# Performance work log

Measured on AMD Instinct MI355X. Metric: run time of the kernel, lower is better.

## Reference

```python
import jax, jax.numpy as jnp
import numpy as np

N = 200000
EPS = 1e-6

def _build_indices():
    # irreps = 128x0e + 64x1e + 32x2e, mirroring MySeperableLayerNorm.__init__ bookkeeping
    scalar_idx = np.arange(128)                       # positions of 0e scalars
    scalar_ch = np.arange(128)                        # their channel ids
    vector_idx = np.arange(128, 480)                  # positions of vector components
    vector_ch_local = np.concatenate([
        np.repeat(np.arange(64), 3),
        np.repeat(np.arange(64, 96), 5),
    ])
    ch_expand = np.concatenate([
        np.arange(128),                               # scalar channels 0..127
        np.repeat(np.arange(128, 192), 3),            # 1e channels 128..191
        np.repeat(np.arange(192, 224), 5),            # 2e channels 192..223
    ])
    return scalar_idx, scalar_ch, vector_idx, vector_ch_local, ch_expand

def setup_inputs() -> dict:
    key = jax.random.key(0)
    ks = jax.random.split(key, 8)
    si, sc, vi, vcl, ce = _build_indices()
    f32 = jnp.float32
    inp = {
        "x": jax.random.normal(ks[0], (N, 480), dtype=f32),
        "W1": jax.random.normal(ks[1], (56, 224), dtype=f32) * 0.05,
        "b1": jax.random.normal(ks[2], (56,), dtype=f32) * 0.05,
        "W2": jax.random.normal(ks[3], (224, 56), dtype=f32) * 0.05,
        "b2": jax.random.normal(ks[4], (224,), dtype=f32) * 0.05,
        "aff_w": 1.0 + 0.1 * jax.random.normal(ks[5], (1, 224), dtype=f32),
        "aff_b": 0.1 * jax.random.normal(ks[6], (1, 128), dtype=f32),
        "scalar_idx": jnp.asarray(si, jnp.int32),
        "scalar_ch": jnp.asarray(sc, jnp.int32),
        "vector_idx": jnp.asarray(vi, jnp.int32),
        "vector_ch_local": jnp.asarray(vcl, jnp.int32),
        "ch_expand": jnp.asarray(ce, jnp.int32),
    }
    return inp

def reference(x, W1, b1, W2, b2, aff_w, aff_b,
              scalar_idx, scalar_ch, vector_idx, vector_ch_local, ch_expand):
    n = x.shape[0]
    num_features = W2.shape[0]
    num_scalar = scalar_idx.shape[0]
    num_vector = num_features - num_scalar

    # --- invariants ---
    scalars = x[:, scalar_idx]                                   # [N, S]
    scalars_centered = scalars - scalars.mean(axis=1, keepdims=True)
    vec_sq = x[:, vector_idx] ** 2                               # [N, Vdim]
    # scatter_mean over vector components -> per-vector mean square
    sums = jnp.zeros((n, num_vector), x.dtype).at[:, vector_ch_local].add(vec_sq)
    counts = jnp.zeros((num_vector,), x.dtype).at[vector_ch_local].add(1.0)
    vectors_rms = jnp.sqrt(sums / counts + EPS)                  # [N, V]

    feats = jnp.concatenate([scalars_centered, vectors_rms], axis=1)  # [N, S+V]
    # gate_norm == 'rms'
    feats = feats * jax.lax.rsqrt(jnp.mean(feats ** 2, axis=1, keepdims=True) + EPS)

    # --- gating MLP (Linear -> SiLU -> Linear) ---
    h = jax.nn.silu(feats @ W1.T + b1)                           # [N, H]
    gate = jax.nn.sigmoid(h @ W2.T + b2) * aff_w                 # [N, C]

    # --- scatter-affine expansion ---
    x_out = x * gate[:, ch_expand]                               # [N, D]
    x_out = x_out.at[:, scalar_idx].set(scalars_centered * gate[:, scalar_ch] + aff_b)
    return x_out
```

## Files before the change

kernel.cpp:

```cpp
#include <hip/hip_runtime.h>

typedef __bf16 bf16;
typedef bf16 bf16x8 __attribute__((ext_vector_type(8)));
typedef float f32x4 __attribute__((ext_vector_type(4)));

#define EPS 1e-6f


__global__ __launch_bounds__(256, 4) void fused(
    const float* __restrict__ x,
    const float* __restrict__ b1v, const float* __restrict__ b2v,
    const float* __restrict__ aw,  const float* __restrict__ ab,
    const bf16* __restrict__ W1b,  const bf16* __restrict__ W2b,
    float* __restrict__ out)
{
    __shared__ unsigned char smem[4 * 7488];
    const int tid = threadIdx.x;
    const int wv  = tid >> 6;
    const int l   = tid & 63;
    const int q   = l >> 4;
    const int c   = l & 15;
    unsigned char* reg = smem + wv * 7488;
    bf16*  feats = (bf16*)reg;
    bf16*  Hs    = (bf16*)reg;
    bf16*  gateb = (bf16*)reg;
    float* srow  = (float*)(reg + 7424);
    const int r0 = blockIdx.x * 64 + wv * 16;

    float cen0[16], cen1[16];
    #pragma unroll
    for (int b = 0; b < 4; ++b) {
        float v0[4], v1[4], t0[4], t1[4], t2[4], p0[4], p1[4], p2[4], p3[4], p4[4];
        #pragma unroll
        for (int j = 0; j < 4; ++j) {
            const float* xr = x + (r0 + 4 * b + j) * 480;
            v0[j] = xr[l];
            v1[j] = xr[64 + l];
            t0[j] = xr[128 + 3 * l];
            t1[j] = xr[129 + 3 * l];
            t2[j] = xr[130 + 3 * l];
            if (l < 32) {
                const float* pp = xr + 320 + 5 * l;
                p0[j] = pp[0]; p1[j] = pp[1]; p2[j] = pp[2]; p3[j] = pp[3]; p4[j] = pp[4];
            }
        }
        #pragma unroll
        for (int j = 0; j < 4; ++j) {
            const int i = 4 * b + j;
            float su = v0[j] + v1[j];
            #pragma unroll
            for (int m = 1; m < 64; m <<= 1) su += __shfl_xor(su, m);
            const float mean = su * (1.0f / 128.0f);
            const float c0 = v0[j] - mean, c1 = v1[j] - mean;
            cen0[i] = c0; cen1[i] = c1;

            const float ra = sqrtf((t0[j]*t0[j] + t1[j]*t1[j] + t2[j]*t2[j]) * (1.0f / 3.0f) + EPS);
            float rb = 0.0f;
            if (l < 32) {
                const float g5 = p0[j]*p0[j] + p1[j]*p1[j] + p2[j]*p2[j] + p3[j]*p3[j] + p4[j]*p4[j];
                rb = sqrtf(g5 * 0.2f + EPS);
            }

            bf16* fr = feats + i * 232;
            fr[l]       = (bf16)c0;
            fr[64 + l]  = (bf16)c1;
            fr[128 + l] = (bf16)ra;
            if (l < 32) fr[192 + l] = (bf16)rb;

            float ms = c0 * c0 + c1 * c1 + ra * ra + rb * rb;
            #pragma unroll
            for (int m = 1; m < 64; m <<= 1) ms += __shfl_xor(ms, m);
            if (l == 0) srow[i] = rsqrtf(ms * (1.0f / 224.0f) + EPS);
        }
    }
    __builtin_amdgcn_wave_barrier();

    bf16x8 af[7];
    {
        const bf16* frow = feats + c * 232;
        #pragma unroll
        for (int ks = 0; ks < 7; ++ks)
            af[ks] = *(const bf16x8*)(frow + ks * 32 + q * 8);
    }
    __builtin_amdgcn_wave_barrier();
    #pragma unroll
    for (int t = 0; t < 4; ++t) {
        f32x4 acc = {0.f, 0.f, 0.f, 0.f};
        const int n = t * 16 + c;
        const bf16* wrow = W1b + n * 224 + q * 8;
        #pragma unroll
        for (int ks = 0; ks < 7; ++ks)
            acc = __builtin_amdgcn_mfma_f32_16x16x32_bf16(
                      af[ks], *(const bf16x8*)(wrow + ks * 32), acc, 0, 0, 0);
        float bb = 0.f;
        if (n < 56) bb = b1v[n];
        #pragma unroll
        for (int r = 0; r < 4; ++r) {
            const int row = q * 4 + r;
            const float z = acc[r] * srow[row] + bb;
            float hv = 0.f;
            if (n < 56) hv = z / (1.f + __expf(-z));
            Hs[row * 72 + n] = (bf16)hv;
        }
    }
    __builtin_amdgcn_wave_barrier();

    const bf16x8 ha0 = *(const bf16x8*)(Hs + c * 72 + q * 8);
    const bf16x8 ha1 = *(const bf16x8*)(Hs + c * 72 + 32 + q * 8);
    __builtin_amdgcn_wave_barrier();
    #pragma unroll
    for (int t = 0; t < 14; ++t) {
        f32x4 acc = {0.f, 0.f, 0.f, 0.f};
        const int nn = t * 16 + c;
        const bf16* wrow = W2b + nn * 64 + q * 8;
        acc = __builtin_amdgcn_mfma_f32_16x16x32_bf16(ha0, *(const bf16x8*)(wrow),      acc, 0, 0, 0);
        acc = __builtin_amdgcn_mfma_f32_16x16x32_bf16(ha1, *(const bf16x8*)(wrow + 32), acc, 0, 0, 0);
        const float bb = b2v[nn];
        const float a  = aw[nn];
        #pragma unroll
        for (int r = 0; r < 4; ++r) {
            const int row = q * 4 + r;
            const float g = a / (1.f + __expf(-(acc[r] + bb)));
            gateb[row * 225 + nn] = (bf16)g;
        }
    }
    __builtin_amdgcn_wave_barrier();

    const float ab0 = ab[l], ab1 = ab[64 + l];
    #pragma unroll
    for (int i = 0; i < 16; ++i) {
        const int base = (r0 + i) * 480;
        const bf16* gr = gateb + i * 225;
        out[base + l]      = cen0[i] * (float)gr[l]      + ab0;
        out[base + 64 + l] = cen1[i] * (float)gr[64 + l] + ab1;
        #pragma unroll
        for (int k = 0; k < 6; ++k) {
            const int cc = 128 + 64 * k + l;
            if (cc < 480) {
                const int d  = cc - 128;
                const int ch = (d < 192) ? (128 + d / 3) : (192 + (d - 192) / 5);
                out[base + cc] = x[base + cc] * (float)gr[ch];
            }
        }
    }
}

__global__ __launch_bounds__(256) void convert_w(
    const float* __restrict__ W1, const float* __restrict__ W2,
    bf16* __restrict__ W1b, bf16* __restrict__ W2b)
{
    const int t = blockIdx.x * 256 + threadIdx.x;
    if (t < 64 * 224) {
        const int n = t / 224, k = t % 224;
        W1b[t] = (n < 56) ? (bf16)W1[n * 224 + k] : (bf16)0.f;
    } else {
        const int u = t - 64 * 224;
        const int n = u >> 6, kk = u & 63;
        W2b[u] = (kk < 56) ? (bf16)W2[n * 56 + kk] : (bf16)0.f;
    }
}

extern "C" void kernel_launch(void* const* d_in, const int* in_sizes, int n_in,
                              void* d_out, int out_size, void* d_ws, size_t ws_size,
                              hipStream_t stream) {
    const float* x  = (const float*)d_in[0];
    const float* W1 = (const float*)d_in[1];
    const float* b1 = (const float*)d_in[2];
    const float* W2 = (const float*)d_in[3];
    const float* b2 = (const float*)d_in[4];
    const float* aw = (const float*)d_in[5];
    const float* ab = (const float*)d_in[6];
    bf16* W1b = (bf16*)d_ws;
    bf16* W2b = W1b + 64 * 224;
    const int rows = in_sizes[0] / 480;
    convert_w<<<112, 256, 0, stream>>>(W1, W2, W1b, W2b);
    fused<<<rows / 64, 256, 0, stream>>>(x, b1, b2, aw, ab, W1b, W2b, (float*)d_out);
}
```

Baseline: 786.4 us.

## Vectorize row loads/stores with 16-lane-per-row mapping and software prefetch

```diff
diff --git a/kernel.cpp b/kernel.cpp
--- a/kernel.cpp
+++ b/kernel.cpp
@@ -2,12 +2,49 @@
 
 typedef __bf16 bf16;
 typedef bf16 bf16x8 __attribute__((ext_vector_type(8)));
+typedef bf16 bf16x4v __attribute__((ext_vector_type(4)));
+typedef bf16 bf16x2v __attribute__((ext_vector_type(2)));
 typedef float f32x4 __attribute__((ext_vector_type(4)));
 
 #define EPS 1e-6f
 
 
-__global__ __launch_bounds__(256, 4) void fused(
+struct XR { float4 s0, s1, t0, t1, t2; float2 u0, u1, u2, u3, u4; };
+struct XE { float4 a0, a1, a2; float2 b0, b1, b2, b3, b4; };
+
+__device__ __forceinline__ XR ldrow(const float* __restrict__ xr, int c) {
+    XR r;
+    r.s0 = *(const float4*)(xr + 8 * c);
+    r.s1 = *(const float4*)(xr + 8 * c + 4);
+    const float* tp = xr + 128 + 12 * c;
+    r.t0 = *(const float4*)(tp);
+    r.t1 = *(const float4*)(tp + 4);
+    r.t2 = *(const float4*)(tp + 8);
+    const float* up = xr + 320 + 10 * c;
+    r.u0 = *(const float2*)(up);
+    r.u1 = *(const float2*)(up + 2);
+    r.u2 = *(const float2*)(up + 4);
+    r.u3 = *(const float2*)(up + 6);
+    r.u4 = *(const float2*)(up + 8);
+    return r;
+}
+
+__device__ __forceinline__ XE ldxe(const float* __restrict__ xr, int c) {
+    XE r;
+    const float* tp = xr + 128 + 12 * c;
+    r.a0 = *(const float4*)(tp);
+    r.a1 = *(const float4*)(tp + 4);
+    r.a2 = *(const float4*)(tp + 8);
+    const float* up = xr + 320 + 10 * c;
+    r.b0 = *(const float2*)(up);
+    r.b1 = *(const float2*)(up + 2);
+    r.b2 = *(const float2*)(up + 4);
+    r.b3 = *(const float2*)(up + 6);
+    r.b4 = *(const float2*)(up + 8);
+    return r;
+}
+
+__global__ __launch_bounds__(256, 5) void fused(
     const float* __restrict__ x,
     const float* __restrict__ b1v, const float* __restrict__ b2v,
     const float* __restrict__ aw,  const float* __restrict__ ab,
@@ -25,53 +62,58 @@
     bf16*  Hs    = (bf16*)reg;
     bf16*  gateb = (bf16*)reg;
     float* srow  = (float*)(reg + 7424);
-    const int r0 = blockIdx.x * 64 + wv * 16;
-
-    float cen0[16], cen1[16];
-    #pragma unroll
-    for (int b = 0; b < 4; ++b) {
-        float v0[4], v1[4], t0[4], t1[4], t2[4], p0[4], p1[4], p2[4], p3[4], p4[4];
-        #pragma unroll
-        for (int j = 0; j < 4; ++j) {
-            const float* xr = x + (r0 + 4 * b + j) * 480;
-            v0[j] = xr[l];
-            v1[j] = xr[64 + l];
-            t0[j] = xr[128 + 3 * l];
-            t1[j] = xr[129 + 3 * l];
-            t2[j] = xr[130 + 3 * l];
-            if (l < 32) {
-                const float* pp = xr + 320 + 5 * l;
-                p0[j] = pp[0]; p1[j] = pp[1]; p2[j] = pp[2]; p3[j] = pp[3]; p4[j] = pp[4];
-            }
-        }
-        #pragma unroll
-        for (int j = 0; j < 4; ++j) {
-            const int i = 4 * b + j;
-            float su = v0[j] + v1[j];
-            #pragma unroll
-            for (int m = 1; m < 64; m <<= 1) su += __shfl_xor(su, m);
-            const float mean = su * (1.0f / 128.0f);
-            const float c0 = v0[j] - mean, c1 = v1[j] - mean;
-            cen0[i] = c0; cen1[i] = c1;
-
-            const float ra = sqrtf((t0[j]*t0[j] + t1[j]*t1[j] + t2[j]*t2[j]) * (1.0f / 3.0f) + EPS);
-            float rb = 0.0f;
-            if (l < 32) {
-                const float g5 = p0[j]*p0[j] + p1[j]*p1[j] + p2[j]*p2[j] + p3[j]*p3[j] + p4[j]*p4[j];
-                rb = sqrtf(g5 * 0.2f + EPS);
-            }
-
-            bf16* fr = feats + i * 232;
-            fr[l]       = (bf16)c0;
-            fr[64 + l]  = (bf16)c1;
-            fr[128 + l] = (bf16)ra;
-            if (l < 32) fr[192 + l] = (bf16)rb;
-
-            float ms = c0 * c0 + c1 * c1 + ra * ra + rb * rb;
-            #pragma unroll
-            for (int m = 1; m < 64; m <<= 1) ms += __shfl_xor(ms, m);
-            if (l == 0) srow[i] = rsqrtf(ms * (1.0f / 224.0f) + EPS);
-        }
+    const int r0w = blockIdx.x * 64 + wv * 16;
+    const float* xw = x + (size_t)r0w * 480;
+
+    float cen[4][8];
+    XR cur = ldrow(xw + q * 480, c);
+    #pragma unroll
+    for (int p = 0; p < 4; ++p) {
+        XR nxt;
+        if (p < 3) nxt = ldrow(xw + (4 * (p + 1) + q) * 480, c);
+        const int i = 4 * p + q;
+        float vs[8] = {cur.s0.x, cur.s0.y, cur.s0.z, cur.s0.w,
+                       cur.s1.x, cur.s1.y, cur.s1.z, cur.s1.w};
+        float S1 = 0.f, SS = 0.f;
+        #pragma unroll
+        for (int j = 0; j < 8; ++j) { S1 += vs[j]; SS = fmaf(vs[j], vs[j], SS); }
+        const float g0 = cur.t0.x*cur.t0.x + cur.t0.y*cur.t0.y + cur.t0.z*cur.t0.z;
+        const float g1 = cur.t0.w*cur.t0.w + cur.t1.x*cur.t1.x + cur.t1.y*cur.t1.y;
+        const float g2 = cur.t1.z*cur.t1.z + cur.t1.w*cur.t1.w + cur.t2.x*cur.t2.x;
+        const float g3 = cur.t2.y*cur.t2.y + cur.t2.z*cur.t2.z + cur.t2.w*cur.t2.w;
+        const float gA = cur.u0.x*cur.u0.x + cur.u0.y*cur.u0.y + cur.u1.x*cur.u1.x
+                       + cur.u1.y*cur.u1.y + cur.u2.x*cur.u2.x;
+        const float gB = cur.u2.y*cur.u2.y + cur.u3.x*cur.u3.x + cur.u3.y*cur.u3.y
+                       + cur.u4.x*cur.u4.x + cur.u4.y*cur.u4.y;
+        float Qp = (g0 + g1 + g2 + g3) * (1.f / 3.f) + (gA + gB) * 0.2f + 6.f * EPS;
+        #pragma unroll
+        for (int m = 1; m < 16; m <<= 1) {
+            S1 += __shfl_xor(S1, m);
+            SS += __shfl_xor(SS, m);
+            Qp += __shfl_xor(Qp, m);
+        }
+        const float mean = S1 * (1.f / 128.f);
+        const float sr = rsqrtf((SS - S1 * mean + Qp) * (1.f / 224.f) + EPS);
+        if (c == 0) srow[i] = sr;
+        bf16x8 fs;
+        #pragma unroll
+        for (int j = 0; j < 8; ++j) {
+            const float cj = vs[j] - mean;
+            cen[p][j] = cj;
+            fs[j] = (bf16)cj;
+        }
+        *(bf16x8*)(feats + i * 232 + 8 * c) = fs;
+        bf16x4v f3;
+        f3[0] = (bf16)sqrtf(g0 * (1.f / 3.f) + EPS);
+        f3[1] = (bf16)sqrtf(g1 * (1.f / 3.f) + EPS);
+        f3[2] = (bf16)sqrtf(g2 * (1.f / 3.f) + EPS);
+        f3[3] = (bf16)sqrtf(g3 * (1.f / 3.f) + EPS);
+        *(bf16x4v*)(feats + i * 232 + 128 + 4 * c) = f3;
+        bf16x2v f5;
+        f5[0] = (bf16)sqrtf(gA * 0.2f + EPS);
+        f5[1] = (bf16)sqrtf(gB * 0.2f + EPS);
+        *(bf16x2v*)(feats + i * 232 + 192 + 2 * c) = f5;
+        if (p < 3) cur = nxt;
     }
     __builtin_amdgcn_wave_barrier();
 
@@ -82,6 +124,9 @@
         for (int ks = 0; ks < 7; ++ks)
             af[ks] = *(const bf16x8*)(frow + ks * 32 + q * 8);
     }
+    float sr4[4];
+    #pragma unroll
+    for (int r = 0; r < 4; ++r) sr4[r] = srow[q * 4 + r];
     __builtin_amdgcn_wave_barrier();
     #pragma unroll
     for (int t = 0; t < 4; ++t) {
@@ -97,7 +142,7 @@
         #pragma unroll
         for (int r = 0; r < 4; ++r) {
             const int row = q * 4 + r;
-            const float z = acc[r] * srow[row] + bb;
+            const float z = acc[r] * sr4[r] + bb;
             float hv = 0.f;
             if (n < 56) hv = z / (1.f + __expf(-z));
             Hs[row * 72 + n] = (bf16)hv;
@@ -107,6 +152,9 @@
 
     const bf16x8 ha0 = *(const bf16x8*)(Hs + c * 72 + q * 8);
     const bf16x8 ha1 = *(const bf16x8*)(Hs + c * 72 + 32 + q * 8);
+    const float4 abA = *(const float4*)(ab + 8 * c);
+    const float4 abB = *(const float4*)(ab + 8 * c + 4);
+    XE xc = ldxe(xw + q * 480, c);
     __builtin_amdgcn_wave_barrier();
     #pragma unroll
     for (int t = 0; t < 14; ++t) {
@@ -121,27 +169,54 @@
         for (int r = 0; r < 4; ++r) {
             const int row = q * 4 + r;
             const float g = a / (1.f + __expf(-(acc[r] + bb)));
-            gateb[row * 225 + nn] = (bf16)g;
-        }
-    }
-    __builtin_amdgcn_wave_barrier();
-
-    const float ab0 = ab[l], ab1 = ab[64 + l];
-    #pragma unroll
-    for (int i = 0; i < 16; ++i) {
-        const int base = (r0 + i) * 480;
-        const bf16* gr = gateb + i * 225;
-        out[base + l]      = cen0[i] * (float)gr[l]      + ab0;
-        out[base + 64 + l] = cen1[i] * (float)gr[64 + l] + ab1;
-        #pragma unroll
-        for (int k = 0; k < 6; ++k) {
-            const int cc = 128 + 64 * k + l;
-            if (cc < 480) {
-                const int d  = cc - 128;
-                const int ch = (d < 192) ? (128 + d / 3) : (192 + (d - 192) / 5);
-                out[base + cc] = x[base + cc] * (float)gr[ch];
-            }
-        }
+            gateb[row * 232 + nn] = (bf16)g;
+        }
+    }
+    __builtin_amdgcn_wave_barrier();
+
+    #pragma unroll
+    for (int p = 0; p < 4; ++p) {
+        const int i = 4 * p + q;
+        XE xn;
+        if (p < 3) xn = ldxe(xw + (i + 4) * 480, c);
+        const bf16x8  gs = *(const bf16x8*)(gateb + i * 232 + 8 * c);
+        const bf16x4v g3 = *(const bf16x4v*)(gateb + i * 232 + 128 + 4 * c);
+        const bf16x2v g5 = *(const bf16x2v*)(gateb + i * 232 + 192 + 2 * c);
+        float* ob = out + (size_t)(r0w + i) * 480;
+        float4 o0, o1;
+        o0.x = fmaf(cen[p][0], (float)gs[0], abA.x);
+        o0.y = fmaf(cen[p][1], (float)gs[1], abA.y);
+        o0.z = fmaf(cen[p][2], (float)gs[2], abA.z);
+        o0.w = fmaf(cen[p][3], (float)gs[3], abA.w);
+        o1.x = fmaf(cen[p][4], (float)gs[4], abB.x);
+        o1.y = fmaf(cen[p][5], (float)gs[5], abB.y);
+        o1.z = fmaf(cen[p][6], (float)gs[6], abB.z);
+        o1.w = fmaf(cen[p][7], (float)gs[7], abB.w);
+        *(float4*)(ob + 8 * c)     = o0;
+        *(float4*)(ob + 8 * c + 4) = o1;
+        const float G0 = (float)g3[0], G1 = (float)g3[1], G2 = (float)g3[2], G3 = (float)g3[3];
+        float4 w0, w1, w2;
+        w0.x = xc.a0.x * G0; w0.y = xc.a0.y * G0; w0.z = xc.a0.z * G0; w0.w = xc.a0.w * G1;
+        w1.x = xc.a1.x * G1; w1.y = xc.a1.y * G1; w1.z = xc.a1.z * G2; w1.w = xc.a1.w * G2;
+        w2.x = xc.a2.x * G2; w2.y = xc.a2.y * G3; w2.z = xc.a2.z * G3; w2.w = xc.a2.w * G3;
+        float* tb = ob + 128 + 12 * c;
+        *(float4*)(tb)     = w0;
+        *(float4*)(tb + 4) = w1;
+        *(float4*)(tb + 8) = w2;
+        const float A = (float)g5[0], B = (float)g5[1];
+        float2 z0, z1, z2, z3, z4;
+        z0.x = xc.b0.x * A; z0.y = xc.b0.y * A;
+        z1.x = xc.b1.x * A; z1.y = xc.b1.y * A;
+        z2.x = xc.b2.x * A; z2.y = xc.b2.y * B;
+        z3.x = xc.b3.x * B; z3.y = xc.b3.y * B;
+        z4.x = xc.b4.x * B; z4.y = xc.b4.y * B;
+        float* ub = ob + 320 + 10 * c;
+        *(float2*)(ub)     = z0;
+        *(float2*)(ub + 2) = z1;
+        *(float2*)(ub + 4) = z2;
+        *(float2*)(ub + 6) = z3;
+        *(float2*)(ub + 8) = z4;
+        if (p < 3) xc = xn;
     }
 }
 
```

Result: slower. 814.7 us (+3.6%).
